# Optimization experiments

Hardware: AMD Instinct MI355X
Metric: run time of the kernel (lower is better)

## Reference

```python
import jax, jax.numpy as jnp
import numpy as np

IN_F = 4096
OUT_F = 11008
N_CLUSTERS = 16
TOPK = int(IN_F * 0.25)  # 1024


def setup_inputs() -> dict:
    key = jax.random.key(0)
    k1, k2, k3, k4 = jax.random.split(key, 4)
    x = jax.random.normal(k1, (1, 1, IN_F), jnp.float32)
    weight_full = jax.random.normal(k2, (OUT_F, IN_F), jnp.float32) * 0.02
    bias_full = jax.random.normal(k3, (OUT_F,), jnp.float32) * 0.02
    # cluster centers live in softmax-activation space (compared via cdist to a softmax)
    cluster_centers = jax.nn.softmax(
        jax.random.normal(k4, (N_CLUSTERS, IN_F), jnp.float32), axis=-1)
    return {"x": x, "weight_full": weight_full, "bias_full": bias_full,
            "cluster_centers": cluster_centers}


def reference(x, weight_full, bias_full, cluster_centers):
    # hot path: bsz * seq == 1
    x_flat = x.reshape(-1, x.shape[-1])                 # [1, in]
    x_avg = jnp.abs(jnp.mean(x_flat, axis=0))           # [in]
    activation = jax.nn.softmax(x_avg, axis=0)          # [in]
    # nearest cluster center (squared L2 has same argmin as L2)
    d2 = jnp.sum((cluster_centers - activation[None, :]) ** 2, axis=-1)  # [n_clusters]
    ci = jnp.argmin(d2)
    center = cluster_centers[ci]                        # [in]
    # per-cluster precomputed top-k column indices: argsort(center, descending)[:topk]
    _, topk_idx = jax.lax.top_k(center, TOPK)           # [topk]
    x_sel = jnp.take(x_flat, topk_idx, axis=1)          # [1, topk]
    w_sel = jnp.take(weight_full, topk_idx, axis=1)     # [out, topk]
    out = x_sel @ w_sel.T + bias_full                   # [1, out]
    return out.reshape(1, 1, -1)
```

## Files before the change

### kernel.cpp

```cpp
#include <hip/hip_runtime.h>

#define IN_F 4096
#define OUT_F 11008
#define NCLUST 16
#define TOPK 1024
#define NT 1024
#define NW 16
#define ROWS_PB 43

typedef float f4 __attribute__((ext_vector_type(4)));

__device__ __forceinline__ float dotf4(f4 a, f4 b) {
    return a[0] * b[0] + a[1] * b[1] + a[2] * b[2] + a[3] * b[3];
}
__device__ __forceinline__ float wredsum(float v) {
    for (int o = 32; o > 0; o >>= 1) v += __shfl_down(v, o, 64);
    return v;
}

__global__ __launch_bounds__(NT) void select_mask_kernel(
    const float* __restrict__ x,
    const float* __restrict__ centers,
    float* __restrict__ xm)
{
    const int tid  = threadIdx.x;
    const int lane = tid & 63;
    const int wid  = tid >> 6;

    __shared__ __align__(16) float sact[IN_F];
    __shared__ unsigned int hist[NW * 256];
    __shared__ float swred[NW];
    __shared__ float sdot[NCLUST], scsq[NCLUST];
    __shared__ unsigned int wtot4[4], weq[NW];
    __shared__ unsigned int sprefix, sKrem, sG;
    __shared__ int sci;

    if (tid == 0) { sprefix = 0u; sKrem = TOPK; sG = 0u; }

    float4 xv = reinterpret_cast<const float4*>(x)[tid];
    float e0 = expf(fabsf(xv.x)), e1 = expf(fabsf(xv.y));
    float e2 = expf(fabsf(xv.z)), e3 = expf(fabsf(xv.w));
    reinterpret_cast<float4*>(sact)[tid] = make_float4(e0, e1, e2, e3);
    {
        float s = wredsum(e0 + e1 + e2 + e3);
        if (lane == 0) swred[wid] = s;
        hist[tid] = 0u; hist[tid + 1024] = 0u;
        hist[tid + 2048] = 0u; hist[tid + 3072] = 0u;
    }
    __syncthreads();
    float S = 0.0f;
    #pragma unroll
    for (int k = 0; k < NW; ++k) S += swred[k];

    {
        const float4* cp = reinterpret_cast<const float4*>(centers + (size_t)wid * IN_F);
        const float4* a4 = reinterpret_cast<const float4*>(sact);
        float dt = 0.0f, cq = 0.0f;
        #pragma unroll
        for (int j = 0; j < 16; ++j) {
            float4 c = cp[j * 64 + lane];
            float4 a = a4[j * 64 + lane];
            dt += c.x * a.x + c.y * a.y + c.z * a.z + c.w * a.w;
            cq += c.x * c.x + c.y * c.y + c.z * c.z + c.w * c.w;
        }
        dt = wredsum(dt);
        cq = wredsum(cq);
        if (lane == 0) { sdot[wid] = dt; scsq[wid] = cq; }
    }
    __syncthreads();

    if (wid == 0) {
        float v = (lane < NCLUST) ? (scsq[lane] - (2.0f / S) * sdot[lane]) : 3.0e38f;
        int bi = lane;
        for (int off = 8; off > 0; off >>= 1) {
            float ov = __shfl_down(v, off, 64);
            int   oi = __shfl_down(bi, off, 64);
            if (ov < v) { v = ov; bi = oi; }
        }
        if (lane == 0) sci = bi;
    }
    __syncthreads();

    unsigned int cv[4];
    {
        float4 c = reinterpret_cast<const float4*>(centers + (size_t)sci * IN_F)[tid];
        cv[0] = __float_as_uint(c.x); cv[1] = __float_as_uint(c.y);
        cv[2] = __float_as_uint(c.z); cv[3] = __float_as_uint(c.w);
    }

    for (int pass = 0; pass < 4; ++pass) {
        const int shift = 24 - 8 * pass;
        const unsigned int pfx  = sprefix;
        const unsigned int krem = sKrem;
        unsigned int* hp = &hist[wid * 256];
        #pragma unroll
        for (int j = 0; j < 4; ++j) {
            unsigned int u = cv[j];
            bool cand = (pass == 0) || ((u >> (shift + 8)) == pfx);
            if (cand) atomicAdd(&hp[(u >> shift) & 255u], 1u);
        }
        __syncthreads();
        unsigned int h = 0, s = 0;
        if (tid < 256) {
            #pragma unroll
            for (int w = 0; w < NW; ++w) { h += hist[w * 256 + tid]; hist[w * 256 + tid] = 0u; }
            s = h;
            for (int off = 1; off < 64; off <<= 1) {
                unsigned int v2 = __shfl_down(s, off, 64);
                if (lane + off < 64) s += v2;
            }
            if (lane == 0) wtot4[wid] = s;
        }
        __syncthreads();
        if (tid < 256) {
            unsigned int add = 0;
            #pragma unroll
            for (int w2 = 0; w2 < 4; ++w2) if (w2 > wid) add += wtot4[w2];
            unsigned int incl = s + add;
            unsigned int excl = incl - h;
            if (excl < krem && krem <= incl) {
                sprefix = (pfx << 8) | (unsigned int)tid;
                sKrem   = krem - excl;
            }
        }
        __syncthreads();
    }
    const unsigned int T = sprefix;

    unsigned int gt = 0, eq = 0;
    #pragma unroll
    for (int j = 0; j < 4; ++j) {
        gt += (cv[j] > T) ? 1u : 0u;
        eq += (cv[j] == T) ? 1u : 0u;
    }
    {
        unsigned int g = gt;
        for (int o = 32; o > 0; o >>= 1) g += __shfl_down(g, o, 64);
        if (lane == 0) atomicAdd(&sG, g);
    }
    unsigned int p = eq;
    for (int off = 1; off < 64; off <<= 1) {
        unsigned int v2 = __shfl_up(p, off, 64);
        if (lane >= off) p += v2;
    }
    if (lane == 63) weq[wid] = p;
    __syncthreads();
    unsigned int base = p - eq;
    #pragma unroll
    for (int w = 0; w < NW; ++w) if (w < wid) base += weq[w];
    const unsigned int needEq = TOPK - sG;

    {
        unsigned int r = 0;
        float4 o;
        o.x = ((cv[0] > T) || ((cv[0] == T) && (base + r < needEq))) ? xv.x : 0.0f; r += (cv[0] == T);
        o.y = ((cv[1] > T) || ((cv[1] == T) && (base + r < needEq))) ? xv.y : 0.0f; r += (cv[1] == T);
        o.z = ((cv[2] > T) || ((cv[2] == T) && (base + r < needEq))) ? xv.z : 0.0f; r += (cv[2] == T);
        o.w = ((cv[3] > T) || ((cv[3] == T) && (base + r < needEq))) ? xv.w : 0.0f;
        reinterpret_cast<float4*>(xm)[tid] = o;
    }
}

__global__ __launch_bounds__(NT) void matvec_kernel(
    const float* __restrict__ W,
    const float* __restrict__ xm,
    const float* __restrict__ bias,
    float* __restrict__ out)
{
    const int tid  = threadIdx.x;
    const int lane = tid & 63;
    const int wid  = tid >> 6;
    const int rbase = blockIdx.x * ROWS_PB;

    __shared__ float spart[ROWS_PB][NW + 1];

    const f4 xv = ((const f4*)xm)[tid];
    const f4* wp = (const f4*)(W + (size_t)rbase * IN_F);

    int r = 0;
    #pragma unroll 2
    for (; r + 4 <= ROWS_PB; r += 4) {
        f4 wa = wp[(size_t)(r + 0) * 1024 + tid];
        f4 wb = wp[(size_t)(r + 1) * 1024 + tid];
        f4 wc = wp[(size_t)(r + 2) * 1024 + tid];
        f4 wd = wp[(size_t)(r + 3) * 1024 + tid];
        float pa = dotf4(wa, xv);
        float pb = dotf4(wb, xv);
        float pc = dotf4(wc, xv);
        float pd = dotf4(wd, xv);
        #pragma unroll
        for (int o = 32; o > 0; o >>= 1) {
            pa += __shfl_down(pa, o, 64);
            pb += __shfl_down(pb, o, 64);
            pc += __shfl_down(pc, o, 64);
            pd += __shfl_down(pd, o, 64);
        }
        if (lane == 0) {
            spart[r + 0][wid] = pa;
            spart[r + 1][wid] = pb;
            spart[r + 2][wid] = pc;
            spart[r + 3][wid] = pd;
        }
    }
    for (; r < ROWS_PB; ++r) {
        f4 w = wp[(size_t)r * 1024 + tid];
        float p = wredsum(dotf4(w, xv));
        if (lane == 0) spart[r][wid] = p;
    }
    __syncthreads();

    if (tid < ROWS_PB) {
        float s = 0.0f;
        #pragma unroll
        for (int w = 0; w < NW; ++w) s += spart[tid][w];
        const int row = rbase + tid;
        out[row] = s + bias[row];
    }
}

extern "C" void kernel_launch(void* const* d_in, const int* in_sizes, int n_in,
                              void* d_out, int out_size, void* d_ws, size_t ws_size,
                              hipStream_t stream) {
    const float* x       = (const float*)d_in[0];
    const float* weight  = (const float*)d_in[1];
    const float* bias    = (const float*)d_in[2];
    const float* centers = (const float*)d_in[3];
    float* out = (float*)d_out;
    float* xm  = (float*)d_ws;

    select_mask_kernel<<<1, NT, 0, stream>>>(x, centers, xm);
    matvec_kernel<<<256, NT, 0, stream>>>(weight, xm, bias, out);
}
```

Before: 43.42 us.

## Split cluster distance computation across blocks and use nontemporal weight loads

Moves the per-cluster dot product and norm computation out of the single-block selection kernel into a separate 16-block kernel, one block per cluster. The single-block kernel then only reads the 32 partial results from the workspace. The goal is to shorten the serial single-block phase, at the cost of one extra kernel launch. Weight loads in the matvec are also switched to nontemporal loads to reduce cache pollution.

```diff
diff --git a/kernel.cpp b/kernel.cpp
--- a/kernel.cpp
+++ b/kernel.cpp
@@ -18,30 +18,59 @@
     return v;
 }
 
-__global__ __launch_bounds__(NT) void select_mask_kernel(
+
+__global__ __launch_bounds__(NT) void cluster_partials_kernel(
     const float* __restrict__ x,
     const float* __restrict__ centers,
-    float* __restrict__ xm)
+    float* __restrict__ ws)
 {
     const int tid  = threadIdx.x;
     const int lane = tid & 63;
     const int wid  = tid >> 6;
-
-    __shared__ __align__(16) float sact[IN_F];
+    const int b    = blockIdx.x;
+
+    __shared__ float sdt[NW], scq[NW];
+
+    f4 xv = ((const f4*)x)[tid];
+    f4 ev;
+    ev[0] = expf(fabsf(xv[0])); ev[1] = expf(fabsf(xv[1]));
+    ev[2] = expf(fabsf(xv[2])); ev[3] = expf(fabsf(xv[3]));
+    f4 cvv = ((const f4*)(centers + (size_t)b * IN_F))[tid];
+
+    float dt = wredsum(dotf4(cvv, ev));
+    float cq = wredsum(dotf4(cvv, cvv));
+    if (lane == 0) { sdt[wid] = dt; scq[wid] = cq; }
+    __syncthreads();
+    if (tid == 0) {
+        float D = 0.0f, Q = 0.0f;
+        #pragma unroll
+        for (int k = 0; k < NW; ++k) { D += sdt[k]; Q += scq[k]; }
+        ws[IN_F + b]      = D;
+        ws[IN_F + 16 + b] = Q;
+    }
+}
+
+__global__ __launch_bounds__(NT) void finalize_mask_kernel(
+    const float* __restrict__ x,
+    const float* __restrict__ centers,
+    float* __restrict__ ws)
+{
+    const int tid  = threadIdx.x;
+    const int lane = tid & 63;
+    const int wid  = tid >> 6;
+
     __shared__ unsigned int hist[NW * 256];
     __shared__ float swred[NW];
-    __shared__ float sdot[NCLUST], scsq[NCLUST];
     __shared__ unsigned int wtot4[4], weq[NW];
     __shared__ unsigned int sprefix, sKrem, sG;
     __shared__ int sci;
 
     if (tid == 0) { sprefix = 0u; sKrem = TOPK; sG = 0u; }
 
-    float4 xv = reinterpret_cast<const float4*>(x)[tid];
-    float e0 = expf(fabsf(xv.x)), e1 = expf(fabsf(xv.y));
-    float e2 = expf(fabsf(xv.z)), e3 = expf(fabsf(xv.w));
-    reinterpret_cast<float4*>(sact)[tid] = make_float4(e0, e1, e2, e3);
-    {
+    f4 xv = ((const f4*)x)[tid];
+    {
+        float e0 = expf(fabsf(xv[0])), e1 = expf(fabsf(xv[1]));
+        float e2 = expf(fabsf(xv[2])), e3 = expf(fabsf(xv[3]));
         float s = wredsum(e0 + e1 + e2 + e3);
         if (lane == 0) swred[wid] = s;
         hist[tid] = 0u; hist[tid + 1024] = 0u;
@@ -52,26 +81,11 @@
     #pragma unroll
     for (int k = 0; k < NW; ++k) S += swred[k];
 
-    {
-        const float4* cp = reinterpret_cast<const float4*>(centers + (size_t)wid * IN_F);
-        const float4* a4 = reinterpret_cast<const float4*>(sact);
-        float dt = 0.0f, cq = 0.0f;
-        #pragma unroll
-        for (int j = 0; j < 16; ++j) {
-            float4 c = cp[j * 64 + lane];
-            float4 a = a4[j * 64 + lane];
-            dt += c.x * a.x + c.y * a.y + c.z * a.z + c.w * a.w;
-            cq += c.x * c.x + c.y * c.y + c.z * c.z + c.w * c.w;
-        }
-        dt = wredsum(dt);
-        cq = wredsum(cq);
-        if (lane == 0) { sdot[wid] = dt; scsq[wid] = cq; }
-    }
-    __syncthreads();
-
     if (wid == 0) {
-        float v = (lane < NCLUST) ? (scsq[lane] - (2.0f / S) * sdot[lane]) : 3.0e38f;
+        float v = 3.0e38f;
         int bi = lane;
+        if (lane < NCLUST)
+            v = ws[IN_F + 16 + lane] - (2.0f / S) * ws[IN_F + lane];
         for (int off = 8; off > 0; off >>= 1) {
             float ov = __shfl_down(v, off, 64);
             int   oi = __shfl_down(bi, off, 64);
@@ -83,9 +97,9 @@
 
     unsigned int cv[4];
     {
-        float4 c = reinterpret_cast<const float4*>(centers + (size_t)sci * IN_F)[tid];
-        cv[0] = __float_as_uint(c.x); cv[1] = __float_as_uint(c.y);
-        cv[2] = __float_as_uint(c.z); cv[3] = __float_as_uint(c.w);
+        f4 c = ((const f4*)(centers + (size_t)sci * IN_F))[tid];
+        cv[0] = __float_as_uint(c[0]); cv[1] = __float_as_uint(c[1]);
+        cv[2] = __float_as_uint(c[2]); cv[3] = __float_as_uint(c[3]);
     }
 
     for (int pass = 0; pass < 4; ++pass) {
@@ -152,12 +166,12 @@
 
     {
         unsigned int r = 0;
-        float4 o;
-        o.x = ((cv[0] > T) || ((cv[0] == T) && (base + r < needEq))) ? xv.x : 0.0f; r += (cv[0] == T);
-        o.y = ((cv[1] > T) || ((cv[1] == T) && (base + r < needEq))) ? xv.y : 0.0f; r += (cv[1] == T);
-        o.z = ((cv[2] > T) || ((cv[2] == T) && (base + r < needEq))) ? xv.z : 0.0f; r += (cv[2] == T);
-        o.w = ((cv[3] > T) || ((cv[3] == T) && (base + r < needEq))) ? xv.w : 0.0f;
-        reinterpret_cast<float4*>(xm)[tid] = o;
+        f4 o;
+        o[0] = ((cv[0] > T) || ((cv[0] == T) && (base + r < needEq))) ? xv[0] : 0.0f; r += (cv[0] == T);
+        o[1] = ((cv[1] > T) || ((cv[1] == T) && (base + r < needEq))) ? xv[1] : 0.0f; r += (cv[1] == T);
+        o[2] = ((cv[2] > T) || ((cv[2] == T) && (base + r < needEq))) ? xv[2] : 0.0f; r += (cv[2] == T);
+        o[3] = ((cv[3] > T) || ((cv[3] == T) && (base + r < needEq))) ? xv[3] : 0.0f;
+        ((f4*)ws)[tid] = o;
     }
 }
 
@@ -180,10 +194,10 @@
     int r = 0;
     #pragma unroll 2
     for (; r + 4 <= ROWS_PB; r += 4) {
-        f4 wa = wp[(size_t)(r + 0) * 1024 + tid];
-        f4 wb = wp[(size_t)(r + 1) * 1024 + tid];
-        f4 wc = wp[(size_t)(r + 2) * 1024 + tid];
-        f4 wd = wp[(size_t)(r + 3) * 1024 + tid];
+        f4 wa = __builtin_nontemporal_load(&wp[(size_t)(r + 0) * 1024 + tid]);
+        f4 wb = __builtin_nontemporal_load(&wp[(size_t)(r + 1) * 1024 + tid]);
+        f4 wc = __builtin_nontemporal_load(&wp[(size_t)(r + 2) * 1024 + tid]);
+        f4 wd = __builtin_nontemporal_load(&wp[(size_t)(r + 3) * 1024 + tid]);
         float pa = dotf4(wa, xv);
         float pb = dotf4(wb, xv);
         float pc = dotf4(wc, xv);
@@ -203,7 +217,7 @@
         }
     }
     for (; r < ROWS_PB; ++r) {
-        f4 w = wp[(size_t)r * 1024 + tid];
+        f4 w = __builtin_nontemporal_load(&wp[(size_t)r * 1024 + tid]);
         float p = wredsum(dotf4(w, xv));
         if (lane == 0) spart[r][wid] = p;
     }
@@ -226,8 +240,9 @@
     const float* bias    = (const float*)d_in[2];
     const float* centers = (const float*)d_in[3];
     float* out = (float*)d_out;
-    float* xm  = (float*)d_ws;
-
-    select_mask_kernel<<<1, NT, 0, stream>>>(x, centers, xm);
-    matvec_kernel<<<256, NT, 0, stream>>>(weight, xm, bias, out);
-}
+    float* ws  = (float*)d_ws;
+
+    cluster_partials_kernel<<<NCLUST, NT, 0, stream>>>(x, centers, ws);
+    finalize_mask_kernel<<<1, NT, 0, stream>>>(x, centers, ws);
+    matvec_kernel<<<256, NT, 0, stream>>>(weight, ws, bias, out);
+}
```

After: 45.51 us. 1.05x slower.
